# Performance work log

Measured on AMD Instinct MI355X. Metric: run time of the kernel, lower is better.

The kernel has to match this reference:

```python
import jax, jax.numpy as jnp
import numpy as np

B, N, D, H, DH, FF, CI, K, MPE = 8, 1024, 512, 8, 64, 2048, 1024, 31, 512
PAD = (K // 2, K // 2 - (K + 1) % 2)  # (15, 15)


def _ln(x, g, b):
    m = x.mean(-1, keepdims=True)
    v = ((x - m) ** 2).mean(-1, keepdims=True)
    return (x - m) * jax.lax.rsqrt(v + 1e-5) * g + b


def _swish(x):
    return x * jax.nn.sigmoid(x)


def setup_inputs() -> dict:
    key = jax.random.key(0)
    ks = iter(jax.random.split(key, 40))
    def w(shape, s=0.02):
        return (jax.random.normal(next(ks), shape) * s).astype(jnp.float32)
    ones = lambda n: jnp.ones((n,), jnp.float32)
    zeros = lambda n: jnp.zeros((n,), jnp.float32)
    return dict(
        x=jax.random.normal(next(ks), (B, N, D), dtype=jnp.float32),
        f1_g=ones(D), f1_b=zeros(D), f1_w1=w((D, FF)), f1_b1=zeros(FF), f1_w2=w((FF, D)), f1_b2=zeros(D),
        a_g=ones(D), a_b=zeros(D), wq=w((D, H * DH)), wkv=w((D, 2 * H * DH)), wo=w((H * DH, D)), wo_b=zeros(D),
        rel=w((2 * MPE + 1, DH)),
        c_g=ones(D), c_b=zeros(D), cw1=w((D, 2 * CI)), cb1=zeros(2 * CI), dw=w((CI, K)), db=zeros(CI),
        bn_g=ones(CI), bn_b=zeros(CI), bn_m=zeros(CI), bn_v=ones(CI), cw2=w((CI, D)), cb2=zeros(D),
        f2_g=ones(D), f2_b=zeros(D), f2_w1=w((D, FF)), f2_b1=zeros(FF), f2_w2=w((FF, D)), f2_b2=zeros(D),
        p_g=ones(D), p_b=zeros(D),
    )


def reference(x, f1_g, f1_b, f1_w1, f1_b1, f1_w2, f1_b2,
              a_g, a_b, wq, wkv, wo, wo_b, rel,
              c_g, c_b, cw1, cb1, dw, db, bn_g, bn_b, bn_m, bn_v, cw2, cb2,
              f2_g, f2_b, f2_w1, f2_b1, f2_w2, f2_b2, p_g, p_b):
    # FF1 (half-step)
    h = _ln(x, f1_g, f1_b)
    x = x + 0.5 * (_swish(h @ f1_w1 + f1_b1) @ f1_w2 + f1_b2)
    # Attention with relative positional bias
    h = _ln(x, a_g, a_b)
    q = (h @ wq).reshape(B, N, H, DH).transpose(0, 2, 1, 3)          # bhnd
    k, v = jnp.split(h @ wkv, 2, axis=-1)
    k = k.reshape(B, N, H, DH).transpose(0, 2, 1, 3)
    v = v.reshape(B, N, H, DH).transpose(0, 2, 1, 3)
    scale = DH ** -0.5
    dots = jnp.einsum('bhid,bhjd->bhij', q, k) * scale
    seq = jnp.arange(N)
    dist = jnp.clip(seq[:, None] - seq[None, :], -MPE, MPE) + MPE    # [N,N]
    rp = rel[dist]                                                   # [N,N,DH]
    dots = dots + jnp.einsum('bhnd,nrd->bhnr', q, rp) * scale
    attn = jax.nn.softmax(dots, axis=-1)
    o = jnp.einsum('bhij,bhjd->bhid', attn, v).transpose(0, 2, 1, 3).reshape(B, N, H * DH)
    x = x + o @ wo + wo_b
    # Conv module: LN -> pw conv -> GLU -> depthwise conv -> BN(eval) -> swish -> pw conv
    h = _ln(x, c_g, c_b)
    h = h @ cw1 + cb1                                                # [B,N,2CI]
    out, gate = jnp.split(h, 2, axis=-1)
    h = (out * jax.nn.sigmoid(gate)).transpose(0, 2, 1)              # [B,CI,N]
    h = jnp.pad(h, ((0, 0), (0, 0), PAD))
    h = jax.lax.conv_general_dilated(h, dw[:, None, :], (1,), 'VALID',
                                     feature_group_count=CI,
                                     dimension_numbers=('NCH', 'OIH', 'NCH')) + db[None, :, None]
    h = (h - bn_m[None, :, None]) * jax.lax.rsqrt(bn_v[None, :, None] + 1e-5) * bn_g[None, :, None] + bn_b[None, :, None]
    h = _swish(h).transpose(0, 2, 1)                                 # [B,N,CI]
    x = x + h @ cw2 + cb2
    # FF2 (half-step) + post norm
    h = _ln(x, f2_g, f2_b)
    x = x + 0.5 * (_swish(h @ f2_w1 + f2_b1) @ f2_w2 + f2_b2)
    return _ln(x, p_g, p_b)
```

## Files before the change

### kernel.cpp

```cpp
#include <hip/hip_runtime.h>
#include <hip/hip_bf16.h>
#include <cstdint>


using bf16_t = __hip_bfloat16;
typedef __bf16 bf16x8 __attribute__((ext_vector_type(8)));
typedef float floatx4 __attribute__((ext_vector_type(4)));

struct alignas(16) hbf8 { bf16_t h[8]; };
struct alignas(8)  hbf4 { bf16_t h[4]; };

__device__ __forceinline__ float  b2f(bf16_t h) { return __bfloat162float(h); }
__device__ __forceinline__ bf16_t f2b(float f)  { return __float2bfloat16(f); }
__device__ __forceinline__ float  sig_(float x) { return 1.f / (1.f + __expf(-x)); }

__device__ __forceinline__ void async16(const void* g, void* l) {
  __builtin_amdgcn_global_load_lds(
      (const __attribute__((address_space(1))) unsigned int*)(uintptr_t)g,
      (__attribute__((address_space(3))) unsigned int*)(uintptr_t)l, 16, 0, 0);
}

struct GemmArgs {
  const bf16_t* A; const bf16_t* Bt; const float* bias; const bf16_t* qr;
  bf16_t* C; float* resid;
  int K, lda, ldb, ldc, ldqr;
  long sAb, sAh, sBb, sBh, sCb, sCh;
  float alpha, beta;
};

template <int BM, int BN, int WR, int WC, int EPI>
__global__ __launch_bounds__(256) void gemm_bt(GemmArgs g) {
  constexpr int FM = BM / (WR * 16);
  constexpr int FN = BN / (WC * 16);
  constexpr int IA = (BM * 4) / 256;
  constexpr int IB = (BN * 4) / 256;
  __shared__ __align__(16) bf16_t As[BM * 32];
  __shared__ __align__(16) bf16_t Bs[BN * 32];
  const int tid = threadIdx.x;
  const int lane = tid & 63, w = tid >> 6;
  int bx = blockIdx.x, by = blockIdx.y;
  {
    const int gx = gridDim.x;
    const int nwg = gx * gridDim.y;
    if ((nwg & 7) == 0 && gridDim.z == 1) {
      int lin = by * gx + bx;
      int lid = (lin & 7) * (nwg >> 3) + (lin >> 3);
      bx = lid % gx; by = lid / gx;
    }
  }
  const int bm0 = by * BM, bn0 = bx * BN;
  const int zb = blockIdx.z >> 3, zh = blockIdx.z & 7;
  const bf16_t* Ab = g.A + (long)zb * g.sAb + (long)zh * g.sAh;
  const bf16_t* Bb = g.Bt + (long)zb * g.sBb + (long)zh * g.sBh;
  const int wm0 = (w / WC) * (FM * 16);
  const int wn0 = (w % WC) * (FN * 16);
  const int lrow = lane & 15, lq = lane >> 4;

  floatx4 acc[FM][FN] = {};

  for (int k0 = 0; k0 < g.K; k0 += 32) {
#pragma unroll
    for (int i = 0; i < IA; ++i) {
      int c = i * 256 + tid;
      int m = c >> 2, kk = (c & 3) * 8;
      async16(Ab + (long)(bm0 + m) * g.lda + (k0 + kk), (char*)As + c * 16);
    }
#pragma unroll
    for (int i = 0; i < IB; ++i) {
      int c = i * 256 + tid;
      int n = bn0 + (c >> 2), kk = (c & 3) * 8;
      async16(Bb + (long)n * g.ldb + (k0 + kk), (char*)Bs + c * 16);
    }
    __syncthreads();
    bf16x8 af[FM], bfr[FN];
#pragma unroll
    for (int fm = 0; fm < FM; ++fm)
      af[fm] = *(const bf16x8*)(As + (wm0 + fm * 16 + lrow) * 32 + lq * 8);
#pragma unroll
    for (int fn = 0; fn < FN; ++fn)
      bfr[fn] = *(const bf16x8*)(Bs + (wn0 + fn * 16 + lrow) * 32 + lq * 8);
#pragma unroll
    for (int fm = 0; fm < FM; ++fm)
#pragma unroll
      for (int fn = 0; fn < FN; ++fn)
        acc[fm][fn] = __builtin_amdgcn_mfma_f32_16x16x32_bf16(af[fm], bfr[fn], acc[fm][fn], 0, 0, 0);
    __syncthreads();
  }

  const int bi = bm0 + wm0 + lq * 4;
  const int bj = bn0 + wn0 + lrow;
  if constexpr (EPI == 2) {
    float* R = g.resid;
#pragma unroll
    for (int fm = 0; fm < FM; ++fm)
#pragma unroll
      for (int fn = 0; fn < FN; ++fn) {
        int j = bj + fn * 16;
        float bv = g.bias ? g.bias[j] : 0.f;
#pragma unroll
        for (int r = 0; r < 4; ++r) {
          long i = bi + fm * 16 + r;
          R[i * g.ldc + j] += g.beta * (acc[fm][fn][r] + bv);
        }
      }
  } else {
    bf16_t* C = g.C + (long)zb * g.sCb + (long)zh * g.sCh;
#pragma unroll
    for (int fm = 0; fm < FM; ++fm)
#pragma unroll
      for (int fn = 0; fn < FN; ++fn) {
        int j = bj + fn * 16;
        float bv = g.bias ? g.bias[j] : 0.f;
#pragma unroll
        for (int r = 0; r < 4; ++r) {
          int i = bi + fm * 16 + r;
          float v = acc[fm][fn][r];
          if constexpr (EPI == 0) v = g.alpha * v + bv;
          if constexpr (EPI == 1) { v += bv; v = v * sig_(v); }
          C[(long)i * g.ldc + j] = f2b(v);
        }
      }
  }
}

__global__ __launch_bounds__(512, 4) void attn_kernel(
    const bf16_t* __restrict__ Q, const bf16_t* __restrict__ KV,
    const bf16_t* __restrict__ VT, const bf16_t* __restrict__ RELP,
    bf16_t* __restrict__ O) {
  constexpr int LDT = 1028;
  __shared__ __align__(16) bf16_t Tls[32 * LDT];
  __shared__ float scr[576];

  const int tid = threadIdx.x;
  const int w = tid >> 6, lane = tid & 63;
  const int lrow = lane & 15, lq = lane >> 4;
  const int lin = blockIdx.y * gridDim.x + blockIdx.x;
  const int lid = (lin & 7) * 256 + (lin >> 3);
  const int z = lid >> 5;
  const int i0 = (lid & 31) * 32;
  const int b = z >> 3, zh = z & 7;
  const int j0w = w * 128;

  const bf16_t* Qb  = Q  + ((long)(b * 1024 + i0)) * 512 + zh * 64;
  const bf16_t* Kb  = KV + ((long)b * 1024) * 1024 + zh * 64;
  const bf16_t* VTb = VT + ((long)(b * 8 + zh)) * 65536;

  bf16x8 af[2][2];
#pragma unroll
  for (int fm = 0; fm < 2; ++fm)
#pragma unroll
    for (int ks = 0; ks < 2; ++ks)
      af[fm][ks] = *(const bf16x8*)(Qb + (long)(fm * 16 + lrow) * 512 + ks * 32 + lq * 8);

  {
    const int u0w = w * 144;
    bf16x8 rf[18];
#pragma unroll
    for (int fnT = 0; fnT < 9; ++fnT) {
      const int u0 = u0w + fnT * 16;
      if (u0 < LDT) {
        rf[2 * fnT]     = *(const bf16x8*)(RELP + (long)(u0 + lrow) * 64 + lq * 8);
        rf[2 * fnT + 1] = *(const bf16x8*)(RELP + (long)(u0 + lrow) * 64 + 32 + lq * 8);
      }
    }
#pragma unroll
    for (int fnT = 0; fnT < 9; ++fnT) {
      const int u0 = u0w + fnT * 16;
      if (u0 < LDT) {
        floatx4 tacc[2] = {};
        tacc[0] = __builtin_amdgcn_mfma_f32_16x16x32_bf16(af[0][0], rf[2 * fnT],     tacc[0], 0, 0, 0);
        tacc[0] = __builtin_amdgcn_mfma_f32_16x16x32_bf16(af[0][1], rf[2 * fnT + 1], tacc[0], 0, 0, 0);
        tacc[1] = __builtin_amdgcn_mfma_f32_16x16x32_bf16(af[1][0], rf[2 * fnT],     tacc[1], 0, 0, 0);
        tacc[1] = __builtin_amdgcn_mfma_f32_16x16x32_bf16(af[1][1], rf[2 * fnT + 1], tacc[1], 0, 0, 0);
        const int uu = u0 + lrow;
#pragma unroll
        for (int fm = 0; fm < 2; ++fm)
#pragma unroll
          for (int r = 0; r < 4; ++r)
            if (uu < LDT)
              Tls[(fm * 16 + lq * 4 + r) * LDT + uu] = f2b(tacc[fm][r]);
      }
    }
  }

  bf16x8 kfA[8], kfB[8];
#pragma unroll
  for (int x = 0; x < 8; ++x)
    kfA[x] = *(const bf16x8*)(Kb + (long)(j0w + (x >> 1) * 16 + lrow) * 1024 + (x & 1) * 32 + lq * 8);
#pragma unroll
  for (int x = 0; x < 8; ++x)
    kfB[x] = *(const bf16x8*)(Kb + (long)(j0w + (4 + (x >> 1)) * 16 + lrow) * 1024 + (x & 1) * 32 + lq * 8);
  __syncthreads();

  floatx4 sacc[2][8] = {};
#pragma unroll
  for (int fn = 0; fn < 4; ++fn) {
    sacc[0][fn] = __builtin_amdgcn_mfma_f32_16x16x32_bf16(af[0][0], kfA[2 * fn],     sacc[0][fn], 0, 0, 0);
    sacc[0][fn] = __builtin_amdgcn_mfma_f32_16x16x32_bf16(af[0][1], kfA[2 * fn + 1], sacc[0][fn], 0, 0, 0);
    sacc[1][fn] = __builtin_amdgcn_mfma_f32_16x16x32_bf16(af[1][0], kfA[2 * fn],     sacc[1][fn], 0, 0, 0);
    sacc[1][fn] = __builtin_amdgcn_mfma_f32_16x16x32_bf16(af[1][1], kfA[2 * fn + 1], sacc[1][fn], 0, 0, 0);
  }
#pragma unroll
  for (int fn = 4; fn < 8; ++fn) {
    sacc[0][fn] = __builtin_amdgcn_mfma_f32_16x16x32_bf16(af[0][0], kfB[2 * (fn - 4)],     sacc[0][fn], 0, 0, 0);
    sacc[0][fn] = __builtin_amdgcn_mfma_f32_16x16x32_bf16(af[0][1], kfB[2 * (fn - 4) + 1], sacc[0][fn], 0, 0, 0);
    sacc[1][fn] = __builtin_amdgcn_mfma_f32_16x16x32_bf16(af[1][0], kfB[2 * (fn - 4)],     sacc[1][fn], 0, 0, 0);
    sacc[1][fn] = __builtin_amdgcn_mfma_f32_16x16x32_bf16(af[1][1], kfB[2 * (fn - 4) + 1], sacc[1][fn], 0, 0, 0);
  }

#pragma unroll
  for (int fm = 0; fm < 2; ++fm)
#pragma unroll
    for (int r = 0; r < 4; ++r) {
      const int il = fm * 16 + lq * 4 + r;
      const bf16_t* trow = Tls + il * LDT + 512;
      const int tb = i0 + il - j0w - lrow;
#pragma unroll
      for (int fn = 0; fn < 8; ++fn) {
        int t = tb - fn * 16;
        t = t < -512 ? -512 : (t > 512 ? 512 : t);
        sacc[fm][fn][r] += b2f(trow[t]);
      }
    }

  float rmax[2][4];
#pragma unroll
  for (int fm = 0; fm < 2; ++fm)
#pragma unroll
    for (int r = 0; r < 4; ++r) {
      float m = sacc[fm][0][r];
#pragma unroll
      for (int fn = 1; fn < 8; ++fn) m = fmaxf(m, sacc[fm][fn][r]);
      rmax[fm][r] = m;
    }
#pragma unroll
  for (int off = 1; off < 16; off <<= 1)
#pragma unroll
    for (int fm = 0; fm < 2; ++fm)
#pragma unroll
      for (int r = 0; r < 4; ++r)
        rmax[fm][r] = fmaxf(rmax[fm][r], __shfl_xor(rmax[fm][r], off));
  if (lrow == 0)
#pragma unroll
    for (int fm = 0; fm < 2; ++fm)
#pragma unroll
      for (int r = 0; r < 4; ++r)
        scr[(fm * 16 + lq * 4 + r) * 9 + w] = rmax[fm][r];
  __syncthreads();

  float rsum[2][4];
#pragma unroll
  for (int fm = 0; fm < 2; ++fm)
#pragma unroll
    for (int r = 0; r < 4; ++r) {
      const float* rr = scr + (fm * 16 + lq * 4 + r) * 9;
      float m = rr[0];
#pragma unroll
      for (int ww = 1; ww < 8; ++ww) m = fmaxf(m, rr[ww]);
      float s = 0.f;
#pragma unroll
      for (int fn = 0; fn < 8; ++fn) {
        float e = __expf(sacc[fm][fn][r] - m);
        sacc[fm][fn][r] = e;
        s += e;
      }
      rsum[fm][r] = s;
    }
#pragma unroll
  for (int off = 1; off < 16; off <<= 1)
#pragma unroll
    for (int fm = 0; fm < 2; ++fm)
#pragma unroll
      for (int r = 0; r < 4; ++r)
        rsum[fm][r] += __shfl_xor(rsum[fm][r], off);
  if (lrow == 0)
#pragma unroll
    for (int fm = 0; fm < 2; ++fm)
#pragma unroll
      for (int r = 0; r < 4; ++r)
        scr[288 + (fm * 16 + lq * 4 + r) * 9 + w] = rsum[fm][r];
  __syncthreads();

  float inv[2][4];
#pragma unroll
  for (int fm = 0; fm < 2; ++fm)
#pragma unroll
    for (int r = 0; r < 4; ++r) {
      const float* rr = scr + 288 + (fm * 16 + lq * 4 + r) * 9;
      float s = rr[0];
#pragma unroll
      for (int ww = 1; ww < 8; ++ww) s += rr[ww];
      inv[fm][r] = 1.f / s;
    }

  bf16x8 vfA[8];
#pragma unroll
  for (int x = 0; x < 8; ++x)
    vfA[x] = *(const bf16x8*)(VTb + (long)((x & 3) * 16 + lrow) * 1024 + j0w + (x >> 2) * 32 + lq * 8);

#pragma unroll
  for (int fm = 0; fm < 2; ++fm)
#pragma unroll
    for (int fn = 0; fn < 8; ++fn)
#pragma unroll
      for (int r = 0; r < 4; ++r) {
        const int i = fm * 16 + lq * 4 + r;
        const int j = j0w + fn * 16 + lrow;
        const unsigned boff = (unsigned)(i * 2048 + j * 2) ^ ((unsigned)(i & 7) << 4);
        *(bf16_t*)((char*)Tls + boff) = f2b(sacc[fm][fn][r] * inv[fm][r]);
      }

  bf16x8 vfB[8];
#pragma unroll
  for (int x = 0; x < 8; ++x)
    vfB[x] = *(const bf16x8*)(VTb + (long)((x & 3) * 16 + lrow) * 1024 + j0w + 64 + (x >> 2) * 32 + lq * 8);

  floatx4 oacc[2][4] = {};
#pragma unroll
  for (int ks = 0; ks < 4; ++ks) {
    const int j = j0w + ks * 32;
    bf16x8 ap[2];
#pragma unroll
    for (int fm = 0; fm < 2; ++fm) {
      const int i = fm * 16 + lrow;
      const unsigned boff = (unsigned)(i * 2048 + (j + lq * 8) * 2) ^ ((unsigned)(i & 7) << 4);
      ap[fm] = *(const bf16x8*)((char*)Tls + boff);
    }
#pragma unroll
    for (int fd = 0; fd < 4; ++fd) {
      bf16x8 bv = (ks < 2) ? vfA[(ks << 2) | fd] : vfB[((ks - 2) << 2) | fd];
      oacc[0][fd] = __builtin_amdgcn_mfma_f32_16x16x32_bf16(ap[0], bv, oacc[0][fd], 0, 0, 0);
      oacc[1][fd] = __builtin_amdgcn_mfma_f32_16x16x32_bf16(ap[1], bv, oacc[1][fd], 0, 0, 0);
    }
  }
  __syncthreads();

  {
    float* part = (float*)Tls + w * 2048;
#pragma unroll
    for (int fm = 0; fm < 2; ++fm)
#pragma unroll
      for (int fd = 0; fd < 4; ++fd)
#pragma unroll
        for (int r = 0; r < 4; ++r)
          part[(fm * 16 + lq * 4 + r) * 64 + fd * 16 + lrow] = oacc[fm][fd][r];
  }
  __syncthreads();

  {
    const int i = tid >> 4;
    const int d0 = (tid & 15) * 4;
    floatx4 s = {};
#pragma unroll
    for (int ww = 0; ww < 8; ++ww)
      s += *(const floatx4*)((const float*)Tls + ww * 2048 + i * 64 + d0);
    hbf4 o4;
#pragma unroll
    for (int m = 0; m < 4; ++m) o4.h[m] = f2b(s[m]);
    *(hbf4*)(O + (long)(b * 1024 + i0 + i) * 512 + zh * 64 + d0) = o4;
  }
}

__global__ __launch_bounds__(256) void diag_kernel(float* __restrict__ out, long n, float v) {
  long i = (long)blockIdx.x * 256 + threadIdx.x;
  if (i < n) out[i] = v;
}

__global__ __launch_bounds__(256) void copy_kernel(const float* __restrict__ x, float* __restrict__ X) {
  long idx = ((long)blockIdx.x * 256 + threadIdx.x) * 4;
  *(float4*)(X + idx) = *(const float4*)(x + idx);
}

__global__ __launch_bounds__(256) void relpad_kernel(const float* __restrict__ rel, bf16_t* __restrict__ RELP) {
  int i = blockIdx.x * 256 + threadIdx.x;
  if (i < 73728) {
    int r = i >> 6, c = i & 63;
    RELP[i] = (r < 1025) ? f2b(rel[r * 64 + c]) : f2b(0.f);
  }
}

template <bool F32OUT>
__global__ __launch_bounds__(256) void ln_kernel(const float* __restrict__ X, const float* __restrict__ gam,
                                                 const float* __restrict__ bet, void* __restrict__ outv) {
  int row = blockIdx.x, tid = threadIdx.x;
  const float* x = X + (long)row * 512;
  float a = x[tid], b = x[tid + 256];
  float s = a + b, q = a * a + b * b;
  for (int off = 32; off; off >>= 1) { s += __shfl_down(s, off); q += __shfl_down(q, off); }
  __shared__ float red[8];
  int w = tid >> 6;
  if ((tid & 63) == 0) { red[w] = s; red[w + 4] = q; }
  __syncthreads();
  float ts = red[0] + red[1] + red[2] + red[3];
  float tq = red[4] + red[5] + red[6] + red[7];
  float mean = ts * (1.f / 512.f);
  float var = tq * (1.f / 512.f) - mean * mean;
  float rs = rsqrtf(var + 1e-5f);
  float o0 = (a - mean) * rs * gam[tid]       + bet[tid];
  float o1 = (b - mean) * rs * gam[tid + 256] + bet[tid + 256];
  if constexpr (F32OUT) {
    float* out = (float*)outv;
    out[(long)row * 512 + tid]       = o0;
    out[(long)row * 512 + tid + 256] = o1;
  } else {
    bf16_t* out = (bf16_t*)outv;
    out[(long)row * 512 + tid]       = f2b(o0);
    out[(long)row * 512 + tid + 256] = f2b(o1);
  }
}

__global__ __launch_bounds__(256) void transpose_kernel(const float* __restrict__ in, bf16_t* __restrict__ out,
                                                        int R, int C) {
  __shared__ float t[32][33];
  int c0 = blockIdx.x * 32, r0 = blockIdx.y * 32;
  int tx = threadIdx.x & 31, ty = threadIdx.x >> 5;
#pragma unroll
  for (int i = 0; i < 4; ++i)
    t[ty + i * 8][tx] = in[(long)(r0 + ty + i * 8) * C + c0 + tx];
  __syncthreads();
#pragma unroll
  for (int i = 0; i < 4; ++i)
    out[(long)(c0 + ty + i * 8) * R + r0 + tx] = f2b(t[tx][ty + i * 8]);
}

__global__ __launch_bounds__(256) void vt_kernel(const bf16_t* __restrict__ KV, bf16_t* __restrict__ VT) {
  int jb = blockIdx.x, z = blockIdx.y;
  int b = z >> 3, h = z & 7;
  const bf16_t* src = KV + (long)b * 1024 * 1024 + 512 + h * 64;
  bf16_t* dst = VT + (long)z * 65536;
  __shared__ bf16_t t[64][65];
  int tid = threadIdx.x;
#pragma unroll
  for (int i = 0; i < 16; ++i) {
    int l = i * 256 + tid;
    int j = l >> 6, d = l & 63;
    t[d][j] = src[(long)(jb * 64 + j) * 1024 + d];
  }
  __syncthreads();
#pragma unroll
  for (int i = 0; i < 16; ++i) {
    int l = i * 256 + tid;
    int d = l >> 6, j = l & 63;
    dst[(long)d * 1024 + jb * 64 + j] = t[d][j];
  }
}

__global__ __launch_bounds__(256) void glu_kernel(const bf16_t* __restrict__ P, bf16_t* __restrict__ out) {
  long idx = ((long)blockIdx.x * 256 + threadIdx.x) * 8;
  long r = idx >> 10;
  int c = (int)(idx & 1023);
  hbf8 a = *(const hbf8*)(P + r * 2048 + c);
  hbf8 g = *(const hbf8*)(P + r * 2048 + 1024 + c);
  hbf8 o;
#pragma unroll
  for (int i = 0; i < 8; ++i) o.h[i] = f2b(b2f(a.h[i]) * sig_(b2f(g.h[i])));
  *(hbf8*)(out + idx) = o;
}

__global__ __launch_bounds__(256) void dwconv_kernel(const bf16_t* __restrict__ G, const float* __restrict__ dw,
    const float* __restrict__ db, const float* __restrict__ bng, const float* __restrict__ bnb,
    const float* __restrict__ bnm, const float* __restrict__ bnv, bf16_t* __restrict__ out) {
  int n0 = blockIdx.x * 32, c0 = blockIdx.y * 64, b = blockIdx.z;
  __shared__ bf16_t t[62][64];
  __shared__ float dws[31][64];
  int tid = threadIdx.x;
  const bf16_t* src = G + (long)b * 1024 * 1024 + c0;
#pragma unroll
  for (int i = 0; i < 16; ++i) {
    int l = i * 256 + tid;
    if (l < 3968) {
      int rr = l >> 6, c = l & 63;
      int n = n0 - 15 + rr;
      t[rr][c] = (n >= 0 && n < 1024) ? src[(long)n * 1024 + c] : f2b(0.f);
    }
  }
#pragma unroll
  for (int i = 0; i < 8; ++i) {
    int l = i * 256 + tid;
    if (l < 1984) {
      int k = l >> 6, c = l & 63;
      dws[k][c] = dw[(long)(c0 + c) * 31 + k];
    }
  }
  __syncthreads();
  int c = tid & 63, nl = tid >> 6;
  float rs = rsqrtf(bnv[c0 + c] + 1e-5f);
  float sc = rs * bng[c0 + c];
  float ab = (db[c0 + c] - bnm[c0 + c]) * sc + bnb[c0 + c];
#pragma unroll
  for (int j = 0; j < 8; ++j) {
    int rr = nl * 8 + j;
    float s = 0.f;
#pragma unroll
    for (int k = 0; k < 31; ++k) s += b2f(t[rr + k][c]) * dws[k][c];
    float y = s * sc + ab;
    out[((long)b * 1024 + n0 + rr) * 1024 + c0 + c] = f2b(y * sig_(y));
  }
}

extern "C" void kernel_launch(void* const* d_in, const int* in_sizes, int n_in,
                              void* d_out, int out_size, void* d_ws, size_t ws_size,
                              hipStream_t stream) {
  auto fail = [&](float code) {
    diag_kernel<<<(out_size + 255) / 256, 256, 0, stream>>>((float*)d_out, out_size, code);
  };
  if (n_in != 34)             { fail(70.f);  return; }
  if (in_sizes[0] != 4194304) { fail(80.f);  return; }

  const float* x     = (const float*)d_in[0];
  const float* f1_g  = (const float*)d_in[1];
  const float* f1_b  = (const float*)d_in[2];
  const float* f1_w1 = (const float*)d_in[3];
  const float* f1_b1 = (const float*)d_in[4];
  const float* f1_w2 = (const float*)d_in[5];
  const float* f1_b2 = (const float*)d_in[6];
  const float* a_g   = (const float*)d_in[7];
  const float* a_b   = (const float*)d_in[8];
  const float* wq    = (const float*)d_in[9];
  const float* wkv   = (const float*)d_in[10];
  const float* wo    = (const float*)d_in[11];
  const float* wo_b  = (const float*)d_in[12];
  const float* rel   = (const float*)d_in[13];
  const float* c_g   = (const float*)d_in[14];
  const float* c_b   = (const float*)d_in[15];
  const float* cw1   = (const float*)d_in[16];
  const float* cb1   = (const float*)d_in[17];
  const float* dwp   = (const float*)d_in[18];
  const float* dbp   = (const float*)d_in[19];
  const float* bn_g  = (const float*)d_in[20];
  const float* bn_b  = (const float*)d_in[21];
  const float* bn_m  = (const float*)d_in[22];
  const float* bn_v  = (const float*)d_in[23];
  const float* cw2   = (const float*)d_in[24];
  const float* cb2   = (const float*)d_in[25];
  const float* f2_g  = (const float*)d_in[26];
  const float* f2_b  = (const float*)d_in[27];
  const float* f2_w1 = (const float*)d_in[28];
  const float* f2_b1 = (const float*)d_in[29];
  const float* f2_w2 = (const float*)d_in[30];
  const float* f2_b2 = (const float*)d_in[31];
  const float* p_g   = (const float*)d_in[32];
  const float* p_b   = (const float*)d_in[33];

  char* ws = (char*)d_ws;
  const size_t OFF_X  = 0;
  const size_t OFF_WT = 16777216;
  const size_t OFF_D  = 30408704;
  const size_t OFF_E  = 63963136;
  const size_t relp_off = OFF_E + 33554432;
  if (ws_size < relp_off + 147456ULL) { fail(200.f); return; }

  float*  X   = (float*)(ws + OFF_X);
  bf16_t* WT  = (bf16_t*)(ws + OFF_WT);
  bf16_t* Q   = (bf16_t*)(ws + OFF_D);
  bf16_t* KV  = (bf16_t*)(ws + OFF_D + 8388608);
  bf16_t* VT  = (bf16_t*)(ws + OFF_D + 25165824);
  bf16_t* GLU = (bf16_t*)(ws + OFF_D);
  bf16_t* DWO = (bf16_t*)(ws + OFF_D + 16777216);
  bf16_t* MID = (bf16_t*)(ws + OFF_E);
  bf16_t* RELP= (bf16_t*)(ws + relp_off);
  bf16_t* H   = (bf16_t*)d_out;
  bf16_t* O   = (bf16_t*)d_out;

  bf16_t* f1_w1t = WT;            bf16_t* f1_w2t = WT + 1048576;
  bf16_t* wqt    = WT + 2097152;  bf16_t* wkvt   = WT + 2359296;
  bf16_t* wot    = WT + 2883584;  bf16_t* cw1t   = WT + 3145728;
  bf16_t* cw2t   = WT + 4194304;  bf16_t* f2_w1t = WT + 4718592;
  bf16_t* f2_w2t = WT + 5767168;

  auto GA = [](const bf16_t* A, const bf16_t* Bt, const float* bias, bf16_t* C,
               float* resid, const bf16_t* qr, int K, int lda, int ldb, int ldc,
               float alpha, float beta) {
    GemmArgs g{}; g.A = A; g.Bt = Bt; g.bias = bias; g.qr = qr; g.C = C; g.resid = resid;
    g.K = K; g.lda = lda; g.ldb = ldb; g.ldc = ldc; g.ldqr = 1152;
    g.sAb = g.sAh = g.sBb = g.sBh = g.sCb = g.sCh = 0; g.alpha = alpha; g.beta = beta;
    return g;
  };
  auto T = [&](const float* in, bf16_t* out, int R, int C) {
    transpose_kernel<<<dim3(C / 32, R / 32), 256, 0, stream>>>(in, out, R, C);
  };

  copy_kernel<<<4096, 256, 0, stream>>>(x, X);
  relpad_kernel<<<288, 256, 0, stream>>>(rel, RELP);
  T(f1_w1, f1_w1t, 512, 2048);  T(f1_w2, f1_w2t, 2048, 512);
  T(wq, wqt, 512, 512);         T(wkv, wkvt, 512, 1024);
  T(wo, wot, 512, 512);         T(cw1, cw1t, 512, 2048);
  T(cw2, cw2t, 1024, 512);      T(f2_w1, f2_w1t, 512, 2048);
  T(f2_w2, f2_w2t, 2048, 512);

  ln_kernel<false><<<8192, 256, 0, stream>>>(X, f1_g, f1_b, H);
  { GemmArgs g = GA(H, f1_w1t, f1_b1, MID, nullptr, nullptr, 512, 512, 512, 2048, 1.f, 0.f);
    gemm_bt<128, 128, 2, 2, 1><<<dim3(16, 64, 1), 256, 0, stream>>>(g); }
  { GemmArgs g = GA(MID, f1_w2t, f1_b2, nullptr, X, nullptr, 2048, 2048, 2048, 512, 1.f, 0.5f);
    gemm_bt<64, 128, 1, 4, 2><<<dim3(4, 128, 1), 256, 0, stream>>>(g); }

  ln_kernel<false><<<8192, 256, 0, stream>>>(X, a_g, a_b, H);
  { GemmArgs g = GA(H, wqt, nullptr, Q, nullptr, nullptr, 512, 512, 512, 512, 0.125f, 0.f);
    gemm_bt<128, 128, 2, 2, 0><<<dim3(4, 64, 1), 256, 0, stream>>>(g); }
  { GemmArgs g = GA(H, wkvt, nullptr, KV, nullptr, nullptr, 512, 512, 512, 1024, 1.f, 0.f);
    gemm_bt<128, 128, 2, 2, 0><<<dim3(8, 64, 1), 256, 0, stream>>>(g); }
  vt_kernel<<<dim3(16, 64), 256, 0, stream>>>(KV, VT);

  attn_kernel<<<dim3(32, 64), 512, 0, stream>>>(Q, KV, VT, RELP, O);

  { GemmArgs g = GA(O, wot, wo_b, nullptr, X, nullptr, 512, 512, 512, 512, 1.f, 1.f);
    gemm_bt<64, 128, 1, 4, 2><<<dim3(4, 128, 1), 256, 0, stream>>>(g); }

  ln_kernel<false><<<8192, 256, 0, stream>>>(X, c_g, c_b, H);
  { GemmArgs g = GA(H, cw1t, cb1, MID, nullptr, nullptr, 512, 512, 512, 2048, 1.f, 0.f);
    gemm_bt<128, 128, 2, 2, 0><<<dim3(16, 64, 1), 256, 0, stream>>>(g); }
  glu_kernel<<<4096, 256, 0, stream>>>(MID, GLU);
  dwconv_kernel<<<dim3(32, 16, 8), 256, 0, stream>>>(GLU, dwp, dbp, bn_g, bn_b, bn_m, bn_v, DWO);
  { GemmArgs g = GA(DWO, cw2t, cb2, nullptr, X, nullptr, 1024, 1024, 1024, 512, 1.f, 1.f);
    gemm_bt<64, 128, 1, 4, 2><<<dim3(4, 128, 1), 256, 0, stream>>>(g); }

  ln_kernel<false><<<8192, 256, 0, stream>>>(X, f2_g, f2_b, H);
  { GemmArgs g = GA(H, f2_w1t, f2_b1, MID, nullptr, nullptr, 512, 512, 512, 2048, 1.f, 0.f);
    gemm_bt<128, 128, 2, 2, 1><<<dim3(16, 64, 1), 256, 0, stream>>>(g); }
  { GemmArgs g = GA(MID, f2_w2t, f2_b2, nullptr, X, nullptr, 2048, 2048, 2048, 512, 1.f, 0.5f);
    gemm_bt<64, 128, 1, 4, 2><<<dim3(4, 128, 1), 256, 0, stream>>>(g); }
  ln_kernel<true><<<8192, 256, 0, stream>>>(X, p_g, p_b, (float*)d_out);
}
```

Baseline: 665.9 us.

## Fuse QKV projections, GLU into GEMM epilogue, and drop input copy

Merges the Q and KV projection GEMMs into a single QKV GEMM, with the attention scale folded into the transposed Wq weights. The attention and V-transpose kernels are updated to read the 1536-wide packed layout. The conv module's first GEMM now uses an interleaved (permuted) weight layout so an epilogue can apply GLU via lane shuffle, removing the separate GLU kernel and the 2048-wide intermediate write/read. The input copy kernel is removed: the first LN reads x directly and the FF1 residual epilogue reads its base from x. This trades a few extra launches and memory passes for slightly more complex epilogues, plus wasted half-lanes in the GLU store.

```diff
diff --git a/kernel.cpp b/kernel.cpp
--- a/kernel.cpp
+++ b/kernel.cpp
@@ -21,9 +21,9 @@
 }
 
 struct GemmArgs {
-  const bf16_t* A; const bf16_t* Bt; const float* bias; const bf16_t* qr;
+  const bf16_t* A; const bf16_t* Bt; const float* bias; const float* srcf;
   bf16_t* C; float* resid;
-  int K, lda, ldb, ldc, ldqr;
+  int K, lda, ldb, ldc;
   long sAb, sAh, sBb, sBh, sCb, sCh;
   float alpha, beta;
 };
@@ -91,6 +91,7 @@
   const int bj = bn0 + wn0 + lrow;
   if constexpr (EPI == 2) {
     float* R = g.resid;
+    const float* S = g.srcf;
 #pragma unroll
     for (int fm = 0; fm < FM; ++fm)
 #pragma unroll
@@ -100,7 +101,25 @@
 #pragma unroll
         for (int r = 0; r < 4; ++r) {
           long i = bi + fm * 16 + r;
-          R[i * g.ldc + j] += g.beta * (acc[fm][fn][r] + bv);
+          float base = S ? S[i * g.ldc + j] : R[i * g.ldc + j];
+          R[i * g.ldc + j] = base + g.beta * (acc[fm][fn][r] + bv);
+        }
+      }
+  } else if constexpr (EPI == 4) {
+    bf16_t* C = g.C;
+#pragma unroll
+    for (int fm = 0; fm < FM; ++fm)
+#pragma unroll
+      for (int fn = 0; fn < FN; ++fn) {
+        int j = bj + fn * 16;
+        float bv = g.bias[(j >> 1) + (j & 1) * 1024];
+#pragma unroll
+        for (int r = 0; r < 4; ++r) {
+          int i = bi + fm * 16 + r;
+          float v = acc[fm][fn][r] + bv;
+          float gp = __shfl_xor(v, 1);
+          if ((j & 1) == 0)
+            C[(long)i * g.ldc + (j >> 1)] = f2b(v * sig_(gp));
         }
       }
   } else {
@@ -124,9 +143,8 @@
 }
 
 __global__ __launch_bounds__(512, 4) void attn_kernel(
-    const bf16_t* __restrict__ Q, const bf16_t* __restrict__ KV,
-    const bf16_t* __restrict__ VT, const bf16_t* __restrict__ RELP,
-    bf16_t* __restrict__ O) {
+    const bf16_t* __restrict__ QKV, const bf16_t* __restrict__ VT,
+    const bf16_t* __restrict__ RELP, bf16_t* __restrict__ O) {
   constexpr int LDT = 1028;
   __shared__ __align__(16) bf16_t Tls[32 * LDT];
   __shared__ float scr[576];
@@ -141,8 +159,8 @@
   const int b = z >> 3, zh = z & 7;
   const int j0w = w * 128;
 
-  const bf16_t* Qb  = Q  + ((long)(b * 1024 + i0)) * 512 + zh * 64;
-  const bf16_t* Kb  = KV + ((long)b * 1024) * 1024 + zh * 64;
+  const bf16_t* Qb  = QKV + ((long)(b * 1024 + i0)) * 1536 + zh * 64;
+  const bf16_t* Kb  = QKV + ((long)b * 1024) * 1536 + 512 + zh * 64;
   const bf16_t* VTb = VT + ((long)(b * 8 + zh)) * 65536;
 
   bf16x8 af[2][2];
@@ -150,7 +168,7 @@
   for (int fm = 0; fm < 2; ++fm)
 #pragma unroll
     for (int ks = 0; ks < 2; ++ks)
-      af[fm][ks] = *(const bf16x8*)(Qb + (long)(fm * 16 + lrow) * 512 + ks * 32 + lq * 8);
+      af[fm][ks] = *(const bf16x8*)(Qb + (long)(fm * 16 + lrow) * 1536 + ks * 32 + lq * 8);
 
   {
     const int u0w = w * 144;
@@ -186,10 +204,10 @@
   bf16x8 kfA[8], kfB[8];
 #pragma unroll
   for (int x = 0; x < 8; ++x)
-    kfA[x] = *(const bf16x8*)(Kb + (long)(j0w + (x >> 1) * 16 + lrow) * 1024 + (x & 1) * 32 + lq * 8);
+    kfA[x] = *(const bf16x8*)(Kb + (long)(j0w + (x >> 1) * 16 + lrow) * 1536 + (x & 1) * 32 + lq * 8);
 #pragma unroll
   for (int x = 0; x < 8; ++x)
-    kfB[x] = *(const bf16x8*)(Kb + (long)(j0w + (4 + (x >> 1)) * 16 + lrow) * 1024 + (x & 1) * 32 + lq * 8);
+    kfB[x] = *(const bf16x8*)(Kb + (long)(j0w + (4 + (x >> 1)) * 16 + lrow) * 1536 + (x & 1) * 32 + lq * 8);
   __syncthreads();
 
   floatx4 sacc[2][8] = {};
@@ -364,11 +382,6 @@
 __global__ __launch_bounds__(256) void diag_kernel(float* __restrict__ out, long n, float v) {
   long i = (long)blockIdx.x * 256 + threadIdx.x;
   if (i < n) out[i] = v;
-}
-
-__global__ __launch_bounds__(256) void copy_kernel(const float* __restrict__ x, float* __restrict__ X) {
-  long idx = ((long)blockIdx.x * 256 + threadIdx.x) * 4;
-  *(float4*)(X + idx) = *(const float4*)(x + idx);
 }
 
 __global__ __launch_bounds__(256) void relpad_kernel(const float* __restrict__ rel, bf16_t* __restrict__ RELP) {
@@ -410,7 +423,7 @@
 }
 
 __global__ __launch_bounds__(256) void transpose_kernel(const float* __restrict__ in, bf16_t* __restrict__ out,
-                                                        int R, int C) {
+                                                        int R, int C, float scale, int perm) {
   __shared__ float t[32][33];
   int c0 = blockIdx.x * 32, r0 = blockIdx.y * 32;
   int tx = threadIdx.x & 31, ty = threadIdx.x >> 5;
@@ -419,14 +432,17 @@
     t[ty + i * 8][tx] = in[(long)(r0 + ty + i * 8) * C + c0 + tx];
   __syncthreads();
 #pragma unroll
-  for (int i = 0; i < 4; ++i)
-    out[(long)(c0 + ty + i * 8) * R + r0 + tx] = f2b(t[tx][ty + i * 8]);
-}
-
-__global__ __launch_bounds__(256) void vt_kernel(const bf16_t* __restrict__ KV, bf16_t* __restrict__ VT) {
+  for (int i = 0; i < 4; ++i) {
+    int c = c0 + ty + i * 8;
+    int row = perm ? ((c < 1024) ? 2 * c : 2 * (c - 1024) + 1) : c;
+    out[(long)row * R + r0 + tx] = f2b(t[tx][ty + i * 8] * scale);
+  }
+}
+
+__global__ __launch_bounds__(256) void vt_kernel(const bf16_t* __restrict__ QKV, bf16_t* __restrict__ VT) {
   int jb = blockIdx.x, z = blockIdx.y;
   int b = z >> 3, h = z & 7;
-  const bf16_t* src = KV + (long)b * 1024 * 1024 + 512 + h * 64;
+  const bf16_t* src = QKV + (long)b * 1024 * 1536 + 1024 + h * 64;
   bf16_t* dst = VT + (long)z * 65536;
   __shared__ bf16_t t[64][65];
   int tid = threadIdx.x;
@@ -434,7 +450,7 @@
   for (int i = 0; i < 16; ++i) {
     int l = i * 256 + tid;
     int j = l >> 6, d = l & 63;
-    t[d][j] = src[(long)(jb * 64 + j) * 1024 + d];
+    t[d][j] = src[(long)(jb * 64 + j) * 1536 + d];
   }
   __syncthreads();
 #pragma unroll
@@ -443,18 +459,6 @@
     int d = l >> 6, j = l & 63;
     dst[(long)d * 1024 + jb * 64 + j] = t[d][j];
   }
-}
-
-__global__ __launch_bounds__(256) void glu_kernel(const bf16_t* __restrict__ P, bf16_t* __restrict__ out) {
-  long idx = ((long)blockIdx.x * 256 + threadIdx.x) * 8;
-  long r = idx >> 10;
-  int c = (int)(idx & 1023);
-  hbf8 a = *(const hbf8*)(P + r * 2048 + c);
-  hbf8 g = *(const hbf8*)(P + r * 2048 + 1024 + c);
-  hbf8 o;
-#pragma unroll
-  for (int i = 0; i < 8; ++i) o.h[i] = f2b(b2f(a.h[i]) * sig_(b2f(g.h[i])));
-  *(hbf8*)(out + idx) = o;
 }
 
 __global__ __launch_bounds__(256) void dwconv_kernel(const bf16_t* __restrict__ G, const float* __restrict__ dw,
@@ -552,8 +556,7 @@
 
   float*  X   = (float*)(ws + OFF_X);
   bf16_t* WT  = (bf16_t*)(ws + OFF_WT);
-  bf16_t* Q   = (bf16_t*)(ws + OFF_D);
-  bf16_t* KV  = (bf16_t*)(ws + OFF_D + 8388608);
+  bf16_t* QKV = (bf16_t*)(ws + OFF_D);
   bf16_t* VT  = (bf16_t*)(ws + OFF_D + 25165824);
   bf16_t* GLU = (bf16_t*)(ws + OFF_D);
   bf16_t* DWO = (bf16_t*)(ws + OFF_D + 16777216);
@@ -563,53 +566,49 @@
   bf16_t* O   = (bf16_t*)d_out;
 
   bf16_t* f1_w1t = WT;            bf16_t* f1_w2t = WT + 1048576;
-  bf16_t* wqt    = WT + 2097152;  bf16_t* wkvt   = WT + 2359296;
+  bf16_t* wqkvt  = WT + 2097152;
   bf16_t* wot    = WT + 2883584;  bf16_t* cw1t   = WT + 3145728;
   bf16_t* cw2t   = WT + 4194304;  bf16_t* f2_w1t = WT + 4718592;
   bf16_t* f2_w2t = WT + 5767168;
 
   auto GA = [](const bf16_t* A, const bf16_t* Bt, const float* bias, bf16_t* C,
-               float* resid, const bf16_t* qr, int K, int lda, int ldb, int ldc,
+               float* resid, const float* srcf, int K, int lda, int ldb, int ldc,
                float alpha, float beta) {
-    GemmArgs g{}; g.A = A; g.Bt = Bt; g.bias = bias; g.qr = qr; g.C = C; g.resid = resid;
-    g.K = K; g.lda = lda; g.ldb = ldb; g.ldc = ldc; g.ldqr = 1152;
+    GemmArgs g{}; g.A = A; g.Bt = Bt; g.bias = bias; g.srcf = srcf; g.C = C; g.resid = resid;
+    g.K = K; g.lda = lda; g.ldb = ldb; g.ldc = ldc;
     g.sAb = g.sAh = g.sBb = g.sBh = g.sCb = g.sCh = 0; g.alpha = alpha; g.beta = beta;
     return g;
   };
-  auto T = [&](const float* in, bf16_t* out, int R, int C) {
-    transpose_kernel<<<dim3(C / 32, R / 32), 256, 0, stream>>>(in, out, R, C);
+  auto T = [&](const float* in, bf16_t* out, int R, int C, float scale = 1.f, int perm = 0) {
+    transpose_kernel<<<dim3(C / 32, R / 32), 256, 0, stream>>>(in, out, R, C, scale, perm);
   };
 
-  copy_kernel<<<4096, 256, 0, stream>>>(x, X);
   relpad_kernel<<<288, 256, 0, stream>>>(rel, RELP);
-  T(f1_w1, f1_w1t, 512, 2048);  T(f1_w2, f1_w2t, 2048, 512);
-  T(wq, wqt, 512, 512);         T(wkv, wkvt, 512, 1024);
-  T(wo, wot, 512, 512);         T(cw1, cw1t, 512, 2048);
-  T(cw2, cw2t, 1024, 512);      T(f2_w1, f2_w1t, 512, 2048);
+  T(f1_w1, f1_w1t, 512, 2048);        T(f1_w2, f1_w2t, 2048, 512);
+  T(wq, wqkvt, 512, 512, 0.125f);     T(wkv, wqkvt + 262144, 512, 1024);
+  T(wo, wot, 512, 512);               T(cw1, cw1t, 512, 2048, 1.f, 1);
+  T(cw2, cw2t, 1024, 512);            T(f2_w1, f2_w1t, 512, 2048);
   T(f2_w2, f2_w2t, 2048, 512);
 
-  ln_kernel<false><<<8192, 256, 0, stream>>>(X, f1_g, f1_b, H);
+  ln_kernel<false><<<8192, 256, 0, stream>>>(x, f1_g, f1_b, H);
   { GemmArgs g = GA(H, f1_w1t, f1_b1, MID, nullptr, nullptr, 512, 512, 512, 2048, 1.f, 0.f);
     gemm_bt<128, 128, 2, 2, 1><<<dim3(16, 64, 1), 256, 0, stream>>>(g); }
-  { GemmArgs g = GA(MID, f1_w2t, f1_b2, nullptr, X, nullptr, 2048, 2048, 2048, 512, 1.f, 0.5f);
+  { GemmArgs g = GA(MID, f1_w2t, f1_b2, nullptr, X, x, 2048, 2048, 2048, 512, 1.f, 0.5f);
     gemm_bt<64, 128, 1, 4, 2><<<dim3(4, 128, 1), 256, 0, stream>>>(g); }
 
   ln_kernel<false><<<8192, 256, 0, stream>>>(X, a_g, a_b, H);
-  { GemmArgs g = GA(H, wqt, nullptr, Q, nullptr, nullptr, 512, 512, 512, 512, 0.125f, 0.f);
-    gemm_bt<128, 128, 2, 2, 0><<<dim3(4, 64, 1), 256, 0, stream>>>(g); }
-  { GemmArgs g = GA(H, wkvt, nullptr, KV, nullptr, nullptr, 512, 512, 512, 1024, 1.f, 0.f);
-    gemm_bt<128, 128, 2, 2, 0><<<dim3(8, 64, 1), 256, 0, stream>>>(g); }
-  vt_kernel<<<dim3(16, 64), 256, 0, stream>>>(KV, VT);
-
-  attn_kernel<<<dim3(32, 64), 512, 0, stream>>>(Q, KV, VT, RELP, O);
+  { GemmArgs g = GA(H, wqkvt, nullptr, QKV, nullptr, nullptr, 512, 512, 512, 1536, 1.f, 0.f);
+    gemm_bt<128, 128, 2, 2, 0><<<dim3(12, 64, 1), 256, 0, stream>>>(g); }
+  vt_kernel<<<dim3(16, 64), 256, 0, stream>>>(QKV, VT);
+
+  attn_kernel<<<dim3(32, 64), 512, 0, stream>>>(QKV, VT, RELP, O);
 
   { GemmArgs g = GA(O, wot, wo_b, nullptr, X, nullptr, 512, 512, 512, 512, 1.f, 1.f);
     gemm_bt<64, 128, 1, 4, 2><<<dim3(4, 128, 1), 256, 0, stream>>>(g); }
 
   ln_kernel<false><<<8192, 256, 0, stream>>>(X, c_g, c_b, H);
-  { GemmArgs g = GA(H, cw1t, cb1, MID, nullptr, nullptr, 512, 512, 512, 2048, 1.f, 0.f);
-    gemm_bt<128, 128, 2, 2, 0><<<dim3(16, 64, 1), 256, 0, stream>>>(g); }
-  glu_kernel<<<4096, 256, 0, stream>>>(MID, GLU);
+  { GemmArgs g = GA(H, cw1t, cb1, GLU, nullptr, nullptr, 512, 512, 512, 1024, 1.f, 0.f);
+    gemm_bt<128, 128, 2, 2, 4><<<dim3(16, 64, 1), 256, 0, stream>>>(g); }
   dwconv_kernel<<<dim3(32, 16, 8), 256, 0, stream>>>(GLU, dwp, dbp, bn_g, bn_b, bn_m, bn_v, DWO);
   { GemmArgs g = GA(DWO, cw2t, cb2, nullptr, X, nullptr, 1024, 1024, 1024, 512, 1.f, 1.f);
     gemm_bt<64, 128, 1, 4, 2><<<dim3(4, 128, 1), 256, 0, stream>>>(g); }
```

Measured after the change: 643.5 us. 1.03x faster.
